# Performance work log

Hardware: AMD Instinct MI355X
Metric: run time of the kernel (lower is better)

The kernel has to match this reference:

```python
import jax, jax.numpy as jnp
import numpy as np

DIM = 256
NUM_HEADS = 8
HEAD_DIM = DIM // NUM_HEADS


def setup_inputs() -> dict:
    key = jax.random.key(0)
    k1, k2, k3, k4 = jax.random.split(key, 4)
    b, n = 4, 2048
    x = jax.random.normal(k1, (b, n, DIM), dtype=jnp.float32)
    # Linear weights with fan-in scaling (matches nn.Linear init magnitude,
    # keeps exp(qk) numerically sane since the original has no max-subtraction).
    Wqkv = jax.random.normal(k2, (DIM, 3 * DIM), dtype=jnp.float32) * (DIM ** -0.5)
    Wout = jax.random.normal(k3, (DIM, DIM), dtype=jnp.float32) * (DIM ** -0.5)
    bout = jax.random.normal(k4, (DIM,), dtype=jnp.float32) * 0.01
    return {"x": x, "Wqkv": Wqkv, "Wout": Wout, "bout": bout}


def reference(x, Wqkv, Wout, bout):
    b, n, d = x.shape
    h, hd = NUM_HEADS, HEAD_DIM
    scale = hd ** -0.5
    qkv = x @ Wqkv  # [b, n, 3d]
    q, k, v = jnp.split(qkv, 3, axis=-1)
    # [b, h, n, hd]
    q = q.reshape(b, n, h, hd).transpose(0, 2, 1, 3) * scale
    k = k.reshape(b, n, h, hd).transpose(0, 2, 1, 3)
    v = v.reshape(b, n, h, hd).transpose(0, 2, 1, 3)
    # Original KeOps path: unnormalized exp (no max-subtraction), separate
    # numerator / denominator reductions, eps in denominator.
    scores = jnp.einsum('bhnd,bhmd->bhnm', q, k)  # [b, h, n, n]
    e = jnp.exp(scores)
    denom = jnp.sum(e, axis=-1, keepdims=True)          # [b, h, n, 1]
    numer = jnp.einsum('bhnm,bhmd->bhnd', e, v)         # [b, h, n, hd]
    out = numer / (denom + 1e-6)
    out = out.transpose(0, 2, 1, 3).reshape(b, n, d)
    return out @ Wout + bout
```

## Files before the change

### kernel.cpp

```cpp
#include <hip/hip_runtime.h>

#define DIM 256
#define NHEADS 8
#define HDIM 32

typedef _Float16 half8_t __attribute__((ext_vector_type(8)));
typedef _Float16 half4_t __attribute__((ext_vector_type(4)));
typedef float float4_t __attribute__((ext_vector_type(4)));

__device__ __forceinline__ void gload_lds16(const void* g, void* l) {
    __builtin_amdgcn_global_load_lds((const __attribute__((address_space(1))) void*)g,
                                     (__attribute__((address_space(3))) void*)l,
                                     16, 0, 0);
}

__global__ __launch_bounds__(256) void prep(const float* __restrict__ x,
                                            const float* __restrict__ Wqkv,
                                            const float* __restrict__ Wout,
                                            _Float16* __restrict__ xh,
                                            _Float16* __restrict__ WqT,
                                            _Float16* __restrict__ WoT) {
    __shared__ float ts[32][33];
    const int bid = blockIdx.x, t = threadIdx.x;
    if (bid < 1024) {
        size_t idx = (size_t)bid * 2048 + (size_t)t * 8;
        float tmp[8];
        *reinterpret_cast<float4*>(tmp)     = *reinterpret_cast<const float4*>(x + idx);
        *reinterpret_cast<float4*>(tmp + 4) = *reinterpret_cast<const float4*>(x + idx + 4);
        half8_t h;
        #pragma unroll
        for (int j = 0; j < 8; ++j) h[j] = (_Float16)tmp[j];
        *reinterpret_cast<half8_t*>(xh + idx) = h;
    } else {
        const float* src; _Float16* dst; int K, N, kb, nb;
        if (bid < 1024 + 192) { int b2 = bid - 1024; src = Wqkv; dst = WqT; K = 256; N = 768; nb = b2 % 24; kb = b2 / 24; }
        else                  { int b3 = bid - 1216; src = Wout; dst = WoT; K = 256; N = 256; nb = b3 % 8;  kb = b3 / 8; }
        const int tx = t & 31, ty = t >> 5;
        #pragma unroll
        for (int i = 0; i < 4; ++i) {
            int k = kb * 32 + ty + i * 8;
            ts[ty + i * 8][tx] = src[(size_t)k * N + nb * 32 + tx];
        }
        __syncthreads();
        #pragma unroll
        for (int i = 0; i < 4; ++i) {
            int nl = ty + i * 8;
            dst[(size_t)(nb * 32 + nl) * K + kb * 32 + tx] = (_Float16)ts[tx][nl];
        }
    }
}

template <bool OUT_HALF, bool VSPLIT>
__global__ __launch_bounds__(256) void gemm_h(const _Float16* __restrict__ A,
                                              const _Float16* __restrict__ BT,
                                              const float* __restrict__ bias,
                                              void* __restrict__ Cv,
                                              _Float16* __restrict__ VTo,
                                              int M, int N, int K, int ldc) {
    __shared__ alignas(16) _Float16 As[128 * 32];
    __shared__ alignas(16) _Float16 Bs[128 * 32];
    const int t = threadIdx.x, lane = t & 63, wave = t >> 6;
    const int l16 = lane & 15, quad = lane >> 4;
    const int m0 = blockIdx.y * 128, n0 = blockIdx.x * 128;
    const int wr = (wave >> 1) * 64, wc = (wave & 1) * 64;
    float4_t acc[4][4];
    #pragma unroll
    for (int i = 0; i < 4; ++i)
        #pragma unroll
        for (int j = 0; j < 4; ++j) acc[i][j] = (float4_t){0.f, 0.f, 0.f, 0.f};

    const int srow = lane >> 2;
    const int scol = (lane & 3) * 8;

    for (int k0 = 0; k0 < K; k0 += 32) {
        #pragma unroll
        for (int i = 0; i < 2; ++i) {
            int chunk = i * 4 + wave;
            int r = chunk * 16 + srow;
            gload_lds16(A  + (size_t)(m0 + r) * K + k0 + scol, As + chunk * 512);
            gload_lds16(BT + (size_t)(n0 + r) * K + k0 + scol, Bs + chunk * 512);
        }
        __syncthreads();
        half8_t af[4], bf[4];
        #pragma unroll
        for (int i = 0; i < 4; ++i)
            af[i] = *reinterpret_cast<const half8_t*>(As + (wr + i * 16 + l16) * 32 + quad * 8);
        #pragma unroll
        for (int j = 0; j < 4; ++j)
            bf[j] = *reinterpret_cast<const half8_t*>(Bs + (wc + j * 16 + l16) * 32 + quad * 8);
        #pragma unroll
        for (int i = 0; i < 4; ++i)
            #pragma unroll
            for (int j = 0; j < 4; ++j)
                acc[i][j] = __builtin_amdgcn_mfma_f32_16x16x32_f16(af[i], bf[j], acc[i][j], 0, 0, 0);
        __syncthreads();
    }

    if (VSPLIT && n0 >= 512) {
        const int bb = m0 >> 11;
        const int tok0 = (m0 & 2047) + wr;
        #pragma unroll
        for (int i = 0; i < 4; ++i)
            #pragma unroll
            for (int j = 0; j < 4; ++j) {
                int vcol = n0 + wc + j * 16 + l16 - 512;
                int hh = vcol >> 5, d = vcol & 31;
                half4_t p;
                #pragma unroll
                for (int r = 0; r < 4; ++r) p[r] = (_Float16)acc[i][j][r];
                *reinterpret_cast<half4_t*>(
                    VTo + ((size_t)(bb * NHEADS + hh) * HDIM + d) * 2048
                        + tok0 + i * 16 + quad * 4) = p;
            }
    } else {
        float bv[4] = {0.f, 0.f, 0.f, 0.f};
        if (bias != nullptr) {
            #pragma unroll
            for (int j = 0; j < 4; ++j) bv[j] = bias[n0 + wc + j * 16 + l16];
        }
        #pragma unroll
        for (int i = 0; i < 4; ++i)
            #pragma unroll
            for (int r = 0; r < 4; ++r) {
                int row = m0 + wr + i * 16 + quad * 4 + r;
                #pragma unroll
                for (int j = 0; j < 4; ++j) {
                    int col = n0 + wc + j * 16 + l16;
                    float v = acc[i][j][r] + bv[j];
                    if (OUT_HALF) ((_Float16*)Cv)[(size_t)row * ldc + col] = (_Float16)v;
                    else          ((float*)Cv)[(size_t)row * ldc + col] = v;
                }
            }
    }
}

__global__ __launch_bounds__(256, 2) void attn_v6(const _Float16* __restrict__ qkh,
                                                  const _Float16* __restrict__ VT,
                                                  _Float16* __restrict__ NUM,
                                                  float* __restrict__ DEN) {
    __shared__ alignas(16) _Float16 es[4][64][40];
    const int bid = blockIdx.x;
    const int kh = bid & 1;
    const int qb = (bid >> 1) & 7;
    const int bh = bid >> 4;
    const int b = bh >> 3, h = bh & 7;
    const int t = threadIdx.x, lane = t & 63, wave = t >> 6;
    const int l16 = lane & 15, quad = lane >> 4;
    const float scale = 0.17677669529663687f;
    const int bN = b * 2048;
    const int q0w = qb * 256 + wave * 64;
    const int kbeg = kh * 1024;

    half8_t qf[4];
    {
        const _Float16* qrow = qkh + (size_t)(bN + q0w + l16) * 512 + h * HDIM + quad * 8;
        #pragma unroll
        for (int g = 0; g < 4; ++g)
            qf[g] = *reinterpret_cast<const half8_t*>(qrow + (size_t)g * 16 * 512);
    }

    const _Float16* kbase = qkh + (size_t)(bN + l16) * 512 + 256 + h * HDIM + quad * 8;
    const _Float16* vbase = VT + (size_t)bh * HDIM * 2048 + (size_t)l16 * 2048 + quad * 8;

    float4_t num[4][2];
    #pragma unroll
    for (int g = 0; g < 4; ++g)
        #pragma unroll
        for (int dt = 0; dt < 2; ++dt) num[g][dt] = (float4_t){0.f, 0.f, 0.f, 0.f};
    float ds[4] = {0.f, 0.f, 0.f, 0.f};
    _Float16* esw = &es[wave][0][0];
    const float4_t z = {0.f, 0.f, 0.f, 0.f};

    for (int k0 = kbeg; k0 < kbeg + 1024; k0 += 64) {
        const _Float16* kp = kbase + (size_t)k0 * 512;
        half8_t kf[4], vf[4];
        #pragma unroll
        for (int j = 0; j < 4; ++j)
            kf[j] = *reinterpret_cast<const half8_t*>(kp + (size_t)j * 16 * 512);
        const _Float16* vp = vbase + k0;
        vf[0] = *reinterpret_cast<const half8_t*>(vp);
        vf[1] = *reinterpret_cast<const half8_t*>(vp + (size_t)16 * 2048);
        vf[2] = *reinterpret_cast<const half8_t*>(vp + 32);
        vf[3] = *reinterpret_cast<const half8_t*>(vp + 32 + (size_t)16 * 2048);

        float4_t st[4][4];
        #pragma unroll
        for (int kb = 0; kb < 4; ++kb)
            #pragma unroll
            for (int g = 0; g < 4; ++g)
                st[kb][g] = __builtin_amdgcn_mfma_f32_16x16x32_f16(kf[kb], qf[g], z, 0, 0, 0);

        half4_t ep[4][4];
        #pragma unroll
        for (int kb = 0; kb < 4; ++kb)
            #pragma unroll
            for (int g = 0; g < 4; ++g)
                #pragma unroll
                for (int r = 0; r < 4; ++r) {
                    float e = __expf(st[kb][g][r] * scale);
                    ds[g] += e;
                    ep[kb][g][r] = (_Float16)e;
                }

        #pragma unroll
        for (int s = 0; s < 2; ++s) {
            #pragma unroll
            for (int tt = 0; tt < 2; ++tt)
                #pragma unroll
                for (int g = 0; g < 4; ++g)
                    *reinterpret_cast<half4_t*>(
                        esw + (g * 16 + l16) * 40 + tt * 16 + quad * 4) = ep[s * 2 + tt][g];

            #pragma unroll
            for (int g = 0; g < 4; ++g) {
                half8_t ef = *reinterpret_cast<const half8_t*>(
                    esw + (g * 16 + l16) * 40 + quad * 8);
                num[g][0] = __builtin_amdgcn_mfma_f32_16x16x32_f16(ef, vf[s * 2],     num[g][0], 0, 0, 0);
                num[g][1] = __builtin_amdgcn_mfma_f32_16x16x32_f16(ef, vf[s * 2 + 1], num[g][1], 0, 0, 0);
            }
        }
    }

    #pragma unroll
    for (int g = 0; g < 4; ++g) {
        ds[g] += __shfl_xor(ds[g], 16, 64);
        ds[g] += __shfl_xor(ds[g], 32, 64);
    }

    _Float16* ob = NUM + (size_t)kh * 2097152 + (size_t)(bN + q0w) * DIM + h * HDIM;
    #pragma unroll
    for (int g = 0; g < 4; ++g)
        #pragma unroll
        for (int r = 0; r < 4; ++r) {
            size_t ro = (size_t)(g * 16 + quad * 4 + r) * DIM;
            ob[ro + l16]      = (_Float16)num[g][0][r];
            ob[ro + 16 + l16] = (_Float16)num[g][1][r];
        }
    if (quad == 0) {
        #pragma unroll
        for (int g = 0; g < 4; ++g)
            DEN[kh * 65536 + bh * 2048 + q0w + g * 16 + l16] = ds[g];
    }
}

__global__ __launch_bounds__(256) void combine(const _Float16* __restrict__ NUM,
                                               const float* __restrict__ DEN,
                                               _Float16* __restrict__ attnh) {
    const size_t idx = ((size_t)blockIdx.x * 256 + threadIdx.x) * 8;
    const int row = (int)(idx >> 8);
    const int c = (int)(idx & 255);
    const int b = row >> 11, tok = row & 2047, h = c >> 5;
    const int di = (b * 8 + h) * 2048 + tok;
    float rcp = 1.0f / (DEN[di] + DEN[di + 65536] + 1e-6f);
    half8_t n0 = *reinterpret_cast<const half8_t*>(NUM + idx);
    half8_t n1 = *reinterpret_cast<const half8_t*>(NUM + idx + 2097152);
    *reinterpret_cast<half8_t*>(attnh + idx) = (n0 + n1) * (_Float16)rcp;
}

extern "C" void kernel_launch(void* const* d_in, const int* in_sizes, int n_in,
                              void* d_out, int out_size, void* d_ws, size_t ws_size,
                              hipStream_t stream) {
    const float* x    = (const float*)d_in[0];
    const float* Wqkv = (const float*)d_in[1];
    const float* Wout = (const float*)d_in[2];
    const float* bout = (const float*)d_in[3];
    float* out = (float*)d_out;
    const int M = 8192;

    _Float16* xh    = (_Float16*)d_ws;
    _Float16* WqT   = xh + (size_t)M * DIM;
    _Float16* WoT   = WqT + 768 * 256;
    _Float16* qkh   = WoT + 256 * 256;
    _Float16* vt    = qkh + (size_t)M * 512;
    _Float16* NUM   = vt + (size_t)32 * HDIM * 2048;
    float*    DEN   = (float*)(NUM + (size_t)2 * M * DIM);
    _Float16* attnh = (_Float16*)(DEN + 2 * 65536);

    hipLaunchKernelGGL(prep, dim3(1280), dim3(256), 0, stream, x, Wqkv, Wout, xh, WqT, WoT);
    hipLaunchKernelGGL((gemm_h<true, true>), dim3(6, 64), dim3(256), 0, stream,
                       xh, WqT, (const float*)nullptr, (void*)qkh, vt, M, 768, DIM, 512);
    hipLaunchKernelGGL(attn_v6, dim3(512), dim3(256), 0, stream, qkh, vt, NUM, DEN);
    hipLaunchKernelGGL(combine, dim3(1024), dim3(256), 0, stream, NUM, DEN, attnh);
    hipLaunchKernelGGL((gemm_h<false, false>), dim3(2, 64), dim3(256), 0, stream,
                       attnh, WoT, bout, (void*)out, (_Float16*)nullptr, M, DIM, DIM, DIM);
}
```

Measured before the change: 125.3 us.

## Pack K/V per head contiguously, shrink QKV GEMM tiles, fuse combine into output GEMM

The QKV projection now writes Q, K and V into separate per-head layouts. K is packed as [bh][tok][32] and V as contiguous 32x32 chunks, so the attention kernel reads them with small-stride loads instead of 1KB-strided rows. The QKV GEMM tile shrinks to 64 rows to launch more blocks. The separate combine kernel is removed: the output GEMM sums the two partial numerators, scales them by the reciprocal denominator while staging A into LDS, and adds the bias. This saves one launch and the attnh round trip, but the A tile now goes through register loads rather than async LDS loads, and the smaller tiles give less reuse.

```diff
diff --git a/kernel.cpp b/kernel.cpp
--- a/kernel.cpp
+++ b/kernel.cpp
@@ -50,22 +50,22 @@
     }
 }
 
-template <bool OUT_HALF, bool VSPLIT>
-__global__ __launch_bounds__(256) void gemm_h(const _Float16* __restrict__ A,
-                                              const _Float16* __restrict__ BT,
-                                              const float* __restrict__ bias,
-                                              void* __restrict__ Cv,
-                                              _Float16* __restrict__ VTo,
-                                              int M, int N, int K, int ldc) {
-    __shared__ alignas(16) _Float16 As[128 * 32];
+__global__ __launch_bounds__(256) void gemm_qkv(const _Float16* __restrict__ A,
+                                                const _Float16* __restrict__ BT,
+                                                _Float16* __restrict__ qh,
+                                                _Float16* __restrict__ kpack,
+                                                _Float16* __restrict__ vp) {
+    __shared__ alignas(16) _Float16 As[64 * 32];
     __shared__ alignas(16) _Float16 Bs[128 * 32];
     const int t = threadIdx.x, lane = t & 63, wave = t >> 6;
     const int l16 = lane & 15, quad = lane >> 4;
-    const int m0 = blockIdx.y * 128, n0 = blockIdx.x * 128;
-    const int wr = (wave >> 1) * 64, wc = (wave & 1) * 64;
-    float4_t acc[4][4];
-    #pragma unroll
-    for (int i = 0; i < 4; ++i)
+    const int m0 = blockIdx.y * 64, n0 = blockIdx.x * 128;
+    const int wr = (wave >> 1) * 32, wc = (wave & 1) * 64;
+    const int K = 256;
+
+    float4_t acc[2][4];
+    #pragma unroll
+    for (int i = 0; i < 2; ++i)
         #pragma unroll
         for (int j = 0; j < 4; ++j) acc[i][j] = (float4_t){0.f, 0.f, 0.f, 0.f};
 
@@ -73,69 +73,72 @@
     const int scol = (lane & 3) * 8;
 
     for (int k0 = 0; k0 < K; k0 += 32) {
-        #pragma unroll
-        for (int i = 0; i < 2; ++i) {
-            int chunk = i * 4 + wave;
-            int r = chunk * 16 + srow;
-            gload_lds16(A  + (size_t)(m0 + r) * K + k0 + scol, As + chunk * 512);
-            gload_lds16(BT + (size_t)(n0 + r) * K + k0 + scol, Bs + chunk * 512);
-        }
-        __syncthreads();
-        half8_t af[4], bf[4];
-        #pragma unroll
-        for (int i = 0; i < 4; ++i)
+        gload_lds16(A  + (size_t)(m0 + wave * 16 + srow) * K + k0 + scol, As + wave * 512);
+        gload_lds16(BT + (size_t)(n0 + wave * 16 + srow) * K + k0 + scol, Bs + wave * 512);
+        gload_lds16(BT + (size_t)(n0 + 64 + wave * 16 + srow) * K + k0 + scol, Bs + 2048 + wave * 512);
+        __syncthreads();
+        half8_t af[2], bf[4];
+        #pragma unroll
+        for (int i = 0; i < 2; ++i)
             af[i] = *reinterpret_cast<const half8_t*>(As + (wr + i * 16 + l16) * 32 + quad * 8);
         #pragma unroll
         for (int j = 0; j < 4; ++j)
             bf[j] = *reinterpret_cast<const half8_t*>(Bs + (wc + j * 16 + l16) * 32 + quad * 8);
         #pragma unroll
-        for (int i = 0; i < 4; ++i)
+        for (int i = 0; i < 2; ++i)
             #pragma unroll
             for (int j = 0; j < 4; ++j)
                 acc[i][j] = __builtin_amdgcn_mfma_f32_16x16x32_f16(af[i], bf[j], acc[i][j], 0, 0, 0);
         __syncthreads();
     }
 
-    if (VSPLIT && n0 >= 512) {
-        const int bb = m0 >> 11;
-        const int tok0 = (m0 & 2047) + wr;
-        #pragma unroll
-        for (int i = 0; i < 4; ++i)
+    const int bb = m0 >> 11;
+    if (n0 < 256) {
+        #pragma unroll
+        for (int i = 0; i < 2; ++i)
+            #pragma unroll
+            for (int r = 0; r < 4; ++r) {
+                int row = m0 + wr + i * 16 + quad * 4 + r;
+                #pragma unroll
+                for (int j = 0; j < 4; ++j)
+                    qh[(size_t)row * 256 + n0 + wc + j * 16 + l16] = (_Float16)acc[i][j][r];
+            }
+    } else if (n0 < 512) {
+        #pragma unroll
+        for (int i = 0; i < 2; ++i)
+            #pragma unroll
+            for (int r = 0; r < 4; ++r) {
+                int tok = (m0 & 2047) + wr + i * 16 + quad * 4 + r;
+                #pragma unroll
+                for (int j = 0; j < 4; ++j) {
+                    int kc = n0 + wc + j * 16 + l16 - 256;
+                    int hh = kc >> 5, dd = kc & 31;
+                    kpack[((size_t)(bb * NHEADS + hh) * 2048 + tok) * 32 + dd] =
+                        (_Float16)acc[i][j][r];
+                }
+            }
+    } else {
+        #pragma unroll
+        for (int i = 0; i < 2; ++i) {
+            int tok0 = (m0 & 2047) + wr + i * 16 + quad * 4;
+            int chunk = tok0 >> 5, tl = tok0 & 31;
             #pragma unroll
             for (int j = 0; j < 4; ++j) {
-                int vcol = n0 + wc + j * 16 + l16 - 512;
-                int hh = vcol >> 5, d = vcol & 31;
+                int vc = n0 + wc + j * 16 + l16 - 512;
+                int hh = vc >> 5, dd = vc & 31;
                 half4_t p;
                 #pragma unroll
                 for (int r = 0; r < 4; ++r) p[r] = (_Float16)acc[i][j][r];
                 *reinterpret_cast<half4_t*>(
-                    VTo + ((size_t)(bb * NHEADS + hh) * HDIM + d) * 2048
-                        + tok0 + i * 16 + quad * 4) = p;
-            }
-    } else {
-        float bv[4] = {0.f, 0.f, 0.f, 0.f};
-        if (bias != nullptr) {
-            #pragma unroll
-            for (int j = 0; j < 4; ++j) bv[j] = bias[n0 + wc + j * 16 + l16];
-        }
-        #pragma unroll
-        for (int i = 0; i < 4; ++i)
-            #pragma unroll
-            for (int r = 0; r < 4; ++r) {
-                int row = m0 + wr + i * 16 + quad * 4 + r;
-                #pragma unroll
-                for (int j = 0; j < 4; ++j) {
-                    int col = n0 + wc + j * 16 + l16;
-                    float v = acc[i][j][r] + bv[j];
-                    if (OUT_HALF) ((_Float16*)Cv)[(size_t)row * ldc + col] = (_Float16)v;
-                    else          ((float*)Cv)[(size_t)row * ldc + col] = v;
-                }
-            }
-    }
-}
-
-__global__ __launch_bounds__(256, 2) void attn_v6(const _Float16* __restrict__ qkh,
-                                                  const _Float16* __restrict__ VT,
+                    vp + (((size_t)(bb * NHEADS + hh) * 64 + chunk) * 32 + dd) * 32 + tl) = p;
+            }
+        }
+    }
+}
+
+__global__ __launch_bounds__(256, 2) void attn_v7(const _Float16* __restrict__ qh,
+                                                  const _Float16* __restrict__ kpack,
+                                                  const _Float16* __restrict__ vp,
                                                   _Float16* __restrict__ NUM,
                                                   float* __restrict__ DEN) {
     __shared__ alignas(16) _Float16 es[4][64][40];
@@ -153,14 +156,14 @@
 
     half8_t qf[4];
     {
-        const _Float16* qrow = qkh + (size_t)(bN + q0w + l16) * 512 + h * HDIM + quad * 8;
+        const _Float16* qrow = qh + (size_t)(bN + q0w + l16) * 256 + h * HDIM + quad * 8;
         #pragma unroll
         for (int g = 0; g < 4; ++g)
-            qf[g] = *reinterpret_cast<const half8_t*>(qrow + (size_t)g * 16 * 512);
-    }
-
-    const _Float16* kbase = qkh + (size_t)(bN + l16) * 512 + 256 + h * HDIM + quad * 8;
-    const _Float16* vbase = VT + (size_t)bh * HDIM * 2048 + (size_t)l16 * 2048 + quad * 8;
+            qf[g] = *reinterpret_cast<const half8_t*>(qrow + (size_t)g * 16 * 256);
+    }
+
+    const _Float16* kb_ = kpack + (size_t)bh * 65536;
+    const _Float16* vb_ = vp + (size_t)bh * 65536;
 
     float4_t num[4][2];
     #pragma unroll
@@ -172,16 +175,18 @@
     const float4_t z = {0.f, 0.f, 0.f, 0.f};
 
     for (int k0 = kbeg; k0 < kbeg + 1024; k0 += 64) {
-        const _Float16* kp = kbase + (size_t)k0 * 512;
         half8_t kf[4], vf[4];
         #pragma unroll
         for (int j = 0; j < 4; ++j)
-            kf[j] = *reinterpret_cast<const half8_t*>(kp + (size_t)j * 16 * 512);
-        const _Float16* vp = vbase + k0;
-        vf[0] = *reinterpret_cast<const half8_t*>(vp);
-        vf[1] = *reinterpret_cast<const half8_t*>(vp + (size_t)16 * 2048);
-        vf[2] = *reinterpret_cast<const half8_t*>(vp + 32);
-        vf[3] = *reinterpret_cast<const half8_t*>(vp + 32 + (size_t)16 * 2048);
+            kf[j] = *reinterpret_cast<const half8_t*>(
+                kb_ + (size_t)(k0 + j * 16 + l16) * 32 + quad * 8);
+        const int c0 = k0 >> 5;
+        #pragma unroll
+        for (int s = 0; s < 2; ++s)
+            #pragma unroll
+            for (int m = 0; m < 2; ++m)
+                vf[s * 2 + m] = *reinterpret_cast<const half8_t*>(
+                    vb_ + ((size_t)(c0 + s) * 32 + m * 16 + l16) * 32 + quad * 8);
 
         float4_t st[4][4];
         #pragma unroll
@@ -243,18 +248,68 @@
     }
 }
 
-__global__ __launch_bounds__(256) void combine(const _Float16* __restrict__ NUM,
-                                               const float* __restrict__ DEN,
-                                               _Float16* __restrict__ attnh) {
-    const size_t idx = ((size_t)blockIdx.x * 256 + threadIdx.x) * 8;
-    const int row = (int)(idx >> 8);
-    const int c = (int)(idx & 255);
-    const int b = row >> 11, tok = row & 2047, h = c >> 5;
-    const int di = (b * 8 + h) * 2048 + tok;
-    float rcp = 1.0f / (DEN[di] + DEN[di + 65536] + 1e-6f);
-    half8_t n0 = *reinterpret_cast<const half8_t*>(NUM + idx);
-    half8_t n1 = *reinterpret_cast<const half8_t*>(NUM + idx + 2097152);
-    *reinterpret_cast<half8_t*>(attnh + idx) = (n0 + n1) * (_Float16)rcp;
+__global__ __launch_bounds__(256) void gemm2c(const _Float16* __restrict__ NUM,
+                                              const float* __restrict__ DEN,
+                                              const _Float16* __restrict__ BT,
+                                              const float* __restrict__ bias,
+                                              float* __restrict__ out) {
+    __shared__ alignas(16) _Float16 As[64 * 32];
+    __shared__ alignas(16) _Float16 Bs[64 * 32];
+    const int t = threadIdx.x, lane = t & 63, wave = t >> 6;
+    const int l16 = lane & 15, quad = lane >> 4;
+    const int m0 = blockIdx.y * 64, n0 = blockIdx.x * 64;
+    const int wr = (wave >> 1) * 32, wc = (wave & 1) * 32;
+    const int bb = m0 >> 11;
+
+    const int arow = t >> 2;
+    const int acol = (t & 3) * 8;
+    const int myrow = m0 + arow;
+    _Float16 rcp8[8];
+    #pragma unroll
+    for (int hh = 0; hh < 8; ++hh) {
+        int di = (bb * 8 + hh) * 2048 + (myrow & 2047);
+        rcp8[hh] = (_Float16)(1.f / (DEN[di] + DEN[di + 65536] + 1e-6f));
+    }
+    const _Float16* np = NUM + (size_t)myrow * 256 + acol;
+
+    float4_t acc[2][2];
+    #pragma unroll
+    for (int i = 0; i < 2; ++i)
+        #pragma unroll
+        for (int j = 0; j < 2; ++j) acc[i][j] = (float4_t){0.f, 0.f, 0.f, 0.f};
+
+    for (int k0 = 0; k0 < 256; k0 += 32) {
+        half8_t n0h = *reinterpret_cast<const half8_t*>(np + k0);
+        half8_t n1h = *reinterpret_cast<const half8_t*>(np + k0 + 2097152);
+        *reinterpret_cast<half8_t*>(As + arow * 32 + acol) = (n0h + n1h) * rcp8[k0 >> 5];
+        gload_lds16(BT + (size_t)(n0 + arow) * 256 + k0 + acol, Bs + t * 8);
+        __syncthreads();
+        half8_t af[2], bf[2];
+        #pragma unroll
+        for (int i = 0; i < 2; ++i)
+            af[i] = *reinterpret_cast<const half8_t*>(As + (wr + i * 16 + l16) * 32 + quad * 8);
+        #pragma unroll
+        for (int j = 0; j < 2; ++j)
+            bf[j] = *reinterpret_cast<const half8_t*>(Bs + (wc + j * 16 + l16) * 32 + quad * 8);
+        #pragma unroll
+        for (int i = 0; i < 2; ++i)
+            #pragma unroll
+            for (int j = 0; j < 2; ++j)
+                acc[i][j] = __builtin_amdgcn_mfma_f32_16x16x32_f16(af[i], bf[j], acc[i][j], 0, 0, 0);
+        __syncthreads();
+    }
+
+    #pragma unroll
+    for (int i = 0; i < 2; ++i)
+        #pragma unroll
+        for (int r = 0; r < 4; ++r) {
+            int row = m0 + wr + i * 16 + quad * 4 + r;
+            #pragma unroll
+            for (int j = 0; j < 2; ++j) {
+                int col = n0 + wc + j * 16 + l16;
+                out[(size_t)row * 256 + col] = acc[i][j][r] + bias[col];
+            }
+        }
 }
 
 extern "C" void kernel_launch(void* const* d_in, const int* in_sizes, int n_in,
@@ -270,17 +325,14 @@
     _Float16* xh    = (_Float16*)d_ws;
     _Float16* WqT   = xh + (size_t)M * DIM;
     _Float16* WoT   = WqT + 768 * 256;
-    _Float16* qkh   = WoT + 256 * 256;
-    _Float16* vt    = qkh + (size_t)M * 512;
-    _Float16* NUM   = vt + (size_t)32 * HDIM * 2048;
+    _Float16* qh    = WoT + 256 * 256;
+    _Float16* kpack = qh + (size_t)M * DIM;
+    _Float16* vp    = kpack + (size_t)32 * 2048 * 32;
+    _Float16* NUM   = vp + (size_t)32 * 2048 * 32;
     float*    DEN   = (float*)(NUM + (size_t)2 * M * DIM);
-    _Float16* attnh = (_Float16*)(DEN + 2 * 65536);
 
     hipLaunchKernelGGL(prep, dim3(1280), dim3(256), 0, stream, x, Wqkv, Wout, xh, WqT, WoT);
-    hipLaunchKernelGGL((gemm_h<true, true>), dim3(6, 64), dim3(256), 0, stream,
-                       xh, WqT, (const float*)nullptr, (void*)qkh, vt, M, 768, DIM, 512);
-    hipLaunchKernelGGL(attn_v6, dim3(512), dim3(256), 0, stream, qkh, vt, NUM, DEN);
-    hipLaunchKernelGGL(combine, dim3(1024), dim3(256), 0, stream, NUM, DEN, attnh);
-    hipLaunchKernelGGL((gemm_h<false, false>), dim3(2, 64), dim3(256), 0, stream,
-                       attnh, WoT, bout, (void*)out, (_Float16*)nullptr, M, DIM, DIM, DIM);
-}
+    hipLaunchKernelGGL(gemm_qkv, dim3(6, 128), dim3(256), 0, stream, xh, WqT, qh, kpack, vp);
+    hipLaunchKernelGGL(attn_v7, dim3(512), dim3(256), 0, stream, qh, kpack, vp, NUM, DEN);
+    hipLaunchKernelGGL(gemm2c, dim3(4, 128), dim3(256), 0, stream, NUM, DEN, WoT, bout, out);
+}
```

Measured after the change: 126.0 us. About the same (+0.6%).
